# Kernel optimization log

Hardware: AMD Instinct MI355X
Metric: run time of the kernel (lower is better)

Reference implementation:

```python
import jax, jax.numpy as jnp
import numpy as np

CAPACITY = 8_388_608  # 2**23, power of two -> leftmost_leaf == capacity
N_UPDATES = 1_048_576  # 2**20


def setup_inputs() -> dict:
    key = jax.random.key(0)
    k1, k2, k3 = jax.random.split(key, 3)
    # Existing tree buffer; values[1] is root, values[CAPACITY:2*CAPACITY] are leaves.
    tree_values = jax.random.uniform(k1, (2 * CAPACITY,), dtype=jnp.float32)
    # Distinct leaf indices in [0, CAPACITY): torch scatter-assign with duplicate
    # indices is nondeterministic, so the meaningful case is distinct indices.
    indices = jax.random.permutation(k2, CAPACITY)[:N_UPDATES].astype(jnp.int32)
    values = jax.random.uniform(k3, (N_UPDATES,), dtype=jnp.float32)
    return {"tree_values": tree_values, "indices": indices, "values": values}


def reference(tree_values, indices, values):
    """SegmentTree.__setitem__ with op=add: set leaves, propagate sums to root.

    Returns the updated (2*capacity,) tree buffer.
    """
    capacity = tree_values.shape[0] // 2  # static python int
    depth = int(capacity).bit_length() - 1  # log2(capacity) levels to the root
    # _index_to_leaf: with power-of-two capacity, leaf = idx + capacity (no wrap).
    leaf = indices.astype(jnp.int32) + capacity
    tree = tree_values.at[leaf].set(values)
    idx = leaf
    # Original does torch.unique(idx//2) per level purely as an optimization;
    # duplicate parents recompute the identical value, so plain scatter-set of
    # op(left_child, right_child) is the same math and jit-friendly.
    for _ in range(depth):
        idx = idx // 2
        parent = tree[2 * idx] + tree[2 * idx + 1]
        tree = tree.at[idx].set(parent)
    return tree
```

## Files before the change

### kernel.cpp

```cpp
#include <hip/hip_runtime.h>


typedef unsigned int uint;
typedef unsigned char uchar;
typedef unsigned long long ull;

#define NBINS 4096
#define FCAP  512

__device__ __forceinline__ ull pc64(ull c) {
    ull x = (c | (c >> 1)) & 0x5555555555555555ull;
    x = (x | (x >> 1))  & 0x3333333333333333ull;
    x = (x | (x >> 2))  & 0x0F0F0F0F0F0F0F0Full;
    x = (x | (x >> 4))  & 0x00FF00FF00FF00FFull;
    x = (x | (x >> 8))  & 0x0000FFFF0000FFFFull;
    x = (x | (x >> 16)) & 0x00000000FFFFFFFFull;
    return x;
}

__global__ void clear_kernel(uint* __restrict__ fcnt) {
    fcnt[blockIdx.x * 256 + threadIdx.x] = 0u;
}

__global__ __launch_bounds__(1024)
void bin_kernel(const int* __restrict__ idx,
                const float* __restrict__ val,
                uint* __restrict__ fcnt,
                uint2* __restrict__ fbins) {
    __shared__ uint hist[NBINS];
    __shared__ uint rbase[NBINS];
    const int tid = threadIdx.x;

    #pragma unroll
    for (int e = 0; e < 4; ++e) hist[e * 1024 + tid] = 0u;
    __syncthreads();

    const int base4 = blockIdx.x * 1024 + tid;
    int4   j4 = ((const int4*)idx)[base4];
    float4 v4 = ((const float4*)val)[base4];
    uint  j[4] = { (uint)j4.x, (uint)j4.y, (uint)j4.z, (uint)j4.w };
    float v[4] = { v4.x, v4.y, v4.z, v4.w };

    #pragma unroll
    for (int e = 0; e < 4; ++e) atomicAdd(&hist[j[e] >> 11], 1u);
    __syncthreads();

    #pragma unroll
    for (int e = 0; e < 4; ++e) {
        int bin = e * 1024 + tid;
        uint h = hist[bin];
        rbase[bin] = h ? atomicAdd(&fcnt[bin], h) : 0u;
        hist[bin] = 0u;
    }
    __syncthreads();

    #pragma unroll
    for (int e = 0; e < 4; ++e) {
        uint bin = j[e] >> 11;
        uint r = rbase[bin] + atomicAdd(&hist[bin], 1u);
        if (r < FCAP)
            fbins[((size_t)bin << 9) + r] =
                make_uint2(j[e] & 2047u, __float_as_uint(v[e]));
    }
}

__global__ __launch_bounds__(256)
void merge_kernel(const float* __restrict__ tree,
                  const uint* __restrict__ fcnt,
                  const uint2* __restrict__ fbins,
                  uchar* __restrict__ l11flag,
                  float* __restrict__ out, int C) {
    __shared__ float slv[2048];
    __shared__ uchar sfl[2048];
    __shared__ float swv[4];
    __shared__ uint  swd[4];

    const int b   = blockIdx.x;
    const int tid = threadIdx.x;
    const int w    = tid >> 6;
    const int lane = tid & 63;

    ((uint2*)sfl)[tid] = make_uint2(0u, 0u);
    __syncthreads();
    uint c = fcnt[b];
    if (c > FCAP) c = FCAP;
    const uint2* mybin = fbins + ((size_t)b << 9);
    for (uint k = tid; k < c; k += 256u) {
        uint2 e = mybin[k];
        uint off = e.x & 2047u;
        slv[off] = __uint_as_float(e.y);
        sfl[off] = 1;
    }
    __syncthreads();

    const int leaf0  = tid * 8;
    const int gleaf0 = b * 2048 + leaf0;

    uint2 fw = *(const uint2*)&sfl[leaf0];
    float4 la = *(const float4*)&slv[leaf0];
    float4 lb = *(const float4*)&slv[leaf0 + 4];
    float4 ta = *(const float4*)(tree + C + gleaf0);
    float4 tb = *(const float4*)(tree + C + gleaf0 + 4);

    float l0 = (fw.x & 0x000000FFu) ? la.x : ta.x;
    float l1 = (fw.x & 0x0000FF00u) ? la.y : ta.y;
    float l2 = (fw.x & 0x00FF0000u) ? la.z : ta.z;
    float l3 = (fw.x & 0xFF000000u) ? la.w : ta.w;
    float l4 = (fw.y & 0x000000FFu) ? lb.x : tb.x;
    float l5 = (fw.y & 0x0000FF00u) ? lb.y : tb.y;
    float l6 = (fw.y & 0x00FF0000u) ? lb.z : tb.z;
    float l7 = (fw.y & 0xFF000000u) ? lb.w : tb.w;

    *(float4*)(out + C + gleaf0)     = make_float4(l0, l1, l2, l3);
    *(float4*)(out + C + gleaf0 + 4) = make_float4(l4, l5, l6, l7);

    uint d10 = (fw.x & 0x0000FFFFu) != 0u;
    uint d11 = (fw.x & 0xFFFF0000u) != 0u;
    uint d12 = (fw.y & 0x0000FFFFu) != 0u;
    uint d13 = (fw.y & 0xFFFF0000u) != 0u;
    float4 t1 = *(const float4*)(tree + (C >> 1) + (gleaf0 >> 1));
    float4 v1;
    v1.x = d10 ? l0 + l1 : t1.x;
    v1.y = d11 ? l2 + l3 : t1.y;
    v1.z = d12 ? l4 + l5 : t1.z;
    v1.w = d13 ? l6 + l7 : t1.w;
    *(float4*)(out + (C >> 1) + (gleaf0 >> 1)) = v1;

    float2 t2 = *(const float2*)(tree + (C >> 2) + (gleaf0 >> 2));
    uint d20 = d10 | d11, d21 = d12 | d13;
    float2 v2;
    v2.x = d20 ? v1.x + v1.y : t2.x;
    v2.y = d21 ? v1.z + v1.w : t2.y;
    *(float2*)(out + (C >> 2) + (gleaf0 >> 2)) = v2;

    float t3 = tree[(C >> 3) + (gleaf0 >> 3)];
    uint d3 = d20 | d21;
    float v = d3 ? v2.x + v2.y : t3;
    out[(C >> 3) + (gleaf0 >> 3)] = v;

    ull m = __ballot(d3 != 0u);
    #pragma unroll
    for (int lvl = 4; lvl <= 9; ++lvl) {
        float a  = __shfl(v, 2 * lane, 64);
        float bb = __shfl(v, 2 * lane + 1, 64);
        m = pc64(m);
        int n = 64 >> (lvl - 3);
        if (lane < n) {
            int node = (C >> lvl) + ((b * 2048 + w * 512) >> lvl) + lane;
            uint d = (uint)(m >> lane) & 1u;
            v = d ? a + bb : tree[node];
            out[node] = v;
        }
    }

    if (lane == 0) { swv[w] = v; swd[w] = (uint)(m & 1ull); }
    __syncthreads();
    if (tid == 0) {
        uint da0 = swd[0] | swd[1], da1 = swd[2] | swd[3];
        int n10 = (C >> 10) + 2 * b;
        float v100 = da0 ? swv[0] + swv[1] : tree[n10];
        float v101 = da1 ? swv[2] + swv[3] : tree[n10 + 1];
        out[n10]     = v100;
        out[n10 + 1] = v101;
        uint d11f = da0 | da1;
        int n11 = (C >> 11) + b;
        out[n11] = d11f ? v100 + v101 : tree[n11];
        l11flag[b] = (uchar)d11f;
    }
}

__global__ __launch_bounds__(1024)
void tail_kernel(const float* __restrict__ tree,
                 const uchar* __restrict__ l11flag,
                 float* __restrict__ out) {
    __shared__ float s16[16];
    __shared__ uint  sd16[16];
    const int t = threadIdx.x, w = t >> 6, lane = t & 63;

    float4 ch = *(const float4*)(out + 4096 + 4 * t);
    uint fl = ((const uint*)l11flag)[t];
    uint d0 = (fl & 0x0000FFFFu) != 0u;
    uint d1 = (fl & 0xFFFF0000u) != 0u;
    float2 t12 = *(const float2*)(tree + 2048 + 2 * t);
    float v0 = d0 ? ch.x + ch.y : t12.x;
    float v1 = d1 ? ch.z + ch.w : t12.y;
    *(float2*)(out + 2048 + 2 * t) = make_float2(v0, v1);
    uint d = d0 | d1;
    float v = d ? v0 + v1 : tree[1024 + t];
    out[1024 + t] = v;

    ull m = __ballot(d != 0u);
    #pragma unroll
    for (int M = 512; M >= 16; M >>= 1) {
        float a  = __shfl(v, 2 * lane, 64);
        float bb = __shfl(v, 2 * lane + 1, 64);
        m = pc64(m);
        int nw = M >> 4;
        if (lane < nw) {
            int node = M + nw * w + lane;
            uint dd = (uint)(m >> lane) & 1u;
            v = dd ? a + bb : tree[node];
            out[node] = v;
        }
    }
    if (lane == 0) { s16[w] = v; sd16[w] = (uint)(m & 1ull); }
    __syncthreads();

    if (w == 0) {
        float vv = lane < 16 ? s16[lane] : 0.f;
        uint dd  = lane < 16 ? sd16[lane] : 0u;
        ull mm = __ballot(dd != 0u);
        #pragma unroll
        for (int M = 8; M >= 1; M >>= 1) {
            float a  = __shfl(vv, 2 * lane, 64);
            float bb = __shfl(vv, 2 * lane + 1, 64);
            mm = pc64(mm);
            if (lane < M) {
                uint d2 = (uint)(mm >> lane) & 1u;
                vv = d2 ? a + bb : tree[M + lane];
                out[M + lane] = vv;
            }
        }
        if (lane == 0) out[0] = tree[0];
    }
}

extern "C" void kernel_launch(void* const* d_in, const int* in_sizes, int n_in,
                              void* d_out, int out_size, void* d_ws, size_t ws_size,
                              hipStream_t stream) {
    const float* tree    = (const float*)d_in[0];
    const int*   indices = (const int*)d_in[1];
    const float* values  = (const float*)d_in[2];
    float* out = (float*)d_out;

    const int two_cap = in_sizes[0];
    const int C       = two_cap >> 1;

    uchar* ws = (uchar*)d_ws;
    uint*  fcnt  = (uint*)ws;
    uchar* l11   = ws + 16384;
    uint2* fbins = (uint2*)(ws + 32768);

    clear_kernel<<<16, 256, 0, stream>>>(fcnt);
    bin_kernel<<<256, 1024, 0, stream>>>(indices, values, fcnt, fbins);
    merge_kernel<<<C / 2048, 256, 0, stream>>>(tree, fcnt, fbins, l11, out, C);
    tail_kernel<<<1, 1024, 0, stream>>>(tree, l11, out);
}
```

Before: 151.0 us.

## Fuse bin, merge and tail into one cooperative kernel with a bitmap

Replaces the clear/bin/merge/tail four-kernel pipeline with a single cooperative kernel that uses grid-wide syncs. Updates are scattered directly into the output leaves and recorded in a global dirty bitmap, which replaces the per-bin histogram and bucket staging. Leaf merging and upward propagation are then done per 512-leaf row, with block 0 finishing the top levels. This removes three kernel launches and the bucket buffer traffic, at the cost of grid.sync barriers, random scattered global writes, and only 256 blocks covering the whole 8M-leaf sweep.

```diff
diff --git a/kernel.cpp b/kernel.cpp
--- a/kernel.cpp
+++ b/kernel.cpp
@@ -1,12 +1,15 @@
 #include <hip/hip_runtime.h>
+#include <hip/hip_cooperative_groups.h>
+
+namespace cg = cooperative_groups;
 
 
 typedef unsigned int uint;
 typedef unsigned char uchar;
 typedef unsigned long long ull;
 
-#define NBINS 4096
-#define FCAP  512
+#define NBLK 256
+#define NTHR 1024
 
 __device__ __forceinline__ ull pc64(ull c) {
     ull x = (c | (c >> 1)) & 0x5555555555555555ull;
@@ -18,210 +21,192 @@
     return x;
 }
 
-__global__ void clear_kernel(uint* __restrict__ fcnt) {
-    fcnt[blockIdx.x * 256 + threadIdx.x] = 0u;
-}
-
-__global__ __launch_bounds__(1024)
-void bin_kernel(const int* __restrict__ idx,
-                const float* __restrict__ val,
-                uint* __restrict__ fcnt,
-                uint2* __restrict__ fbins) {
-    __shared__ uint hist[NBINS];
-    __shared__ uint rbase[NBINS];
-    const int tid = threadIdx.x;
-
-    #pragma unroll
-    for (int e = 0; e < 4; ++e) hist[e * 1024 + tid] = 0u;
-    __syncthreads();
-
-    const int base4 = blockIdx.x * 1024 + tid;
-    int4   j4 = ((const int4*)idx)[base4];
-    float4 v4 = ((const float4*)val)[base4];
-    uint  j[4] = { (uint)j4.x, (uint)j4.y, (uint)j4.z, (uint)j4.w };
-    float v[4] = { v4.x, v4.y, v4.z, v4.w };
-
-    #pragma unroll
-    for (int e = 0; e < 4; ++e) atomicAdd(&hist[j[e] >> 11], 1u);
-    __syncthreads();
-
-    #pragma unroll
-    for (int e = 0; e < 4; ++e) {
-        int bin = e * 1024 + tid;
-        uint h = hist[bin];
-        rbase[bin] = h ? atomicAdd(&fcnt[bin], h) : 0u;
-        hist[bin] = 0u;
+__global__ __launch_bounds__(NTHR)
+void fused_kernel(const float* __restrict__ tree,
+                  const int* __restrict__ idx,
+                  const float* __restrict__ val,
+                  uint* __restrict__ bitmap,
+                  uchar* __restrict__ l9flag,
+                  float* __restrict__ out,
+                  int C, int nupd) {
+    cg::grid_group grid = cg::this_grid();
+    const int tid  = threadIdx.x;
+    const int b    = blockIdx.x;
+    const int gtid = b * NTHR + tid;
+
+    if (gtid < (C >> 5)) bitmap[gtid] = 0u;
+    __threadfence();
+    grid.sync();
+
+    if (4 * gtid < nupd) {
+        int4   j4 = ((const int4*)idx)[gtid];
+        float4 v4 = ((const float4*)val)[gtid];
+        out[C + j4.x] = v4.x;
+        out[C + j4.y] = v4.y;
+        out[C + j4.z] = v4.z;
+        out[C + j4.w] = v4.w;
+        atomicOr(&bitmap[((uint)j4.x) >> 5], 1u << (((uint)j4.x) & 31u));
+        atomicOr(&bitmap[((uint)j4.y) >> 5], 1u << (((uint)j4.y) & 31u));
+        atomicOr(&bitmap[((uint)j4.z) >> 5], 1u << (((uint)j4.z) & 31u));
+        atomicOr(&bitmap[((uint)j4.w) >> 5], 1u << (((uint)j4.w) & 31u));
     }
-    __syncthreads();
-
-    #pragma unroll
-    for (int e = 0; e < 4; ++e) {
-        uint bin = j[e] >> 11;
-        uint r = rbase[bin] + atomicAdd(&hist[bin], 1u);
-        if (r < FCAP)
-            fbins[((size_t)bin << 9) + r] =
-                make_uint2(j[e] & 2047u, __float_as_uint(v[e]));
+    __threadfence();
+    grid.sync();
+
+    {
+        const int wv   = tid >> 6;
+        const int lane = tid & 63;
+        #pragma unroll
+        for (int it = 0; it < 4; ++it) {
+            const int r      = b * 64 + it * 16 + wv;
+            const int gleaf0 = r * 512 + lane * 8;
+            uint dm = (uint)((const uchar*)bitmap)[r * 64 + lane];
+
+            float4 ta = *(const float4*)(tree + C + gleaf0);
+            float4 tb = *(const float4*)(tree + C + gleaf0 + 4);
+            float4 oa = make_float4(0.f, 0.f, 0.f, 0.f), ob = oa;
+            if (dm) {
+                oa = *(const float4*)(out + C + gleaf0);
+                ob = *(const float4*)(out + C + gleaf0 + 4);
+            }
+            float l0 = (dm &   1u) ? oa.x : ta.x;
+            float l1 = (dm &   2u) ? oa.y : ta.y;
+            float l2 = (dm &   4u) ? oa.z : ta.z;
+            float l3 = (dm &   8u) ? oa.w : ta.w;
+            float l4 = (dm &  16u) ? ob.x : tb.x;
+            float l5 = (dm &  32u) ? ob.y : tb.y;
+            float l6 = (dm &  64u) ? ob.z : tb.z;
+            float l7 = (dm & 128u) ? ob.w : tb.w;
+            *(float4*)(out + C + gleaf0)     = make_float4(l0, l1, l2, l3);
+            *(float4*)(out + C + gleaf0 + 4) = make_float4(l4, l5, l6, l7);
+
+            uint d10 = dm & 3u, d11 = dm & 12u, d12 = dm & 48u, d13 = dm & 192u;
+            float4 t1 = *(const float4*)(tree + (C >> 1) + (gleaf0 >> 1));
+            float4 v1;
+            v1.x = d10 ? l0 + l1 : t1.x;
+            v1.y = d11 ? l2 + l3 : t1.y;
+            v1.z = d12 ? l4 + l5 : t1.z;
+            v1.w = d13 ? l6 + l7 : t1.w;
+            *(float4*)(out + (C >> 1) + (gleaf0 >> 1)) = v1;
+
+            float2 t2 = *(const float2*)(tree + (C >> 2) + (gleaf0 >> 2));
+            uint d20 = d10 | d11, d21 = d12 | d13;
+            float2 v2;
+            v2.x = d20 ? v1.x + v1.y : t2.x;
+            v2.y = d21 ? v1.z + v1.w : t2.y;
+            *(float2*)(out + (C >> 2) + (gleaf0 >> 2)) = v2;
+
+            float t3v = tree[(C >> 3) + (gleaf0 >> 3)];
+            uint d3 = d20 | d21;
+            float v = d3 ? v2.x + v2.y : t3v;
+            out[(C >> 3) + (gleaf0 >> 3)] = v;
+
+            ull m = __ballot(d3 != 0u);
+            #pragma unroll
+            for (int lvl = 4; lvl <= 9; ++lvl) {
+                float a  = __shfl(v, 2 * lane, 64);
+                float bb = __shfl(v, 2 * lane + 1, 64);
+                m = pc64(m);
+                int n = 64 >> (lvl - 3);
+                if (lane < n) {
+                    int node = (C >> lvl) + (r << (9 - lvl)) + lane;
+                    uint dd = (uint)(m >> lane) & 1u;
+                    v = dd ? a + bb : tree[node];
+                    out[node] = v;
+                }
+            }
+            if (lane == 0) l9flag[r] = (uchar)(m & 1ull);
+        }
     }
-}
-
-__global__ __launch_bounds__(256)
-void merge_kernel(const float* __restrict__ tree,
-                  const uint* __restrict__ fcnt,
-                  const uint2* __restrict__ fbins,
-                  uchar* __restrict__ l11flag,
-                  float* __restrict__ out, int C) {
-    __shared__ float slv[2048];
-    __shared__ uchar sfl[2048];
-    __shared__ float swv[4];
-    __shared__ uint  swd[4];
-
-    const int b   = blockIdx.x;
-    const int tid = threadIdx.x;
-    const int w    = tid >> 6;
-    const int lane = tid & 63;
-
-    ((uint2*)sfl)[tid] = make_uint2(0u, 0u);
-    __syncthreads();
-    uint c = fcnt[b];
-    if (c > FCAP) c = FCAP;
-    const uint2* mybin = fbins + ((size_t)b << 9);
-    for (uint k = tid; k < c; k += 256u) {
-        uint2 e = mybin[k];
-        uint off = e.x & 2047u;
-        slv[off] = __uint_as_float(e.y);
-        sfl[off] = 1;
-    }
-    __syncthreads();
-
-    const int leaf0  = tid * 8;
-    const int gleaf0 = b * 2048 + leaf0;
-
-    uint2 fw = *(const uint2*)&sfl[leaf0];
-    float4 la = *(const float4*)&slv[leaf0];
-    float4 lb = *(const float4*)&slv[leaf0 + 4];
-    float4 ta = *(const float4*)(tree + C + gleaf0);
-    float4 tb = *(const float4*)(tree + C + gleaf0 + 4);
-
-    float l0 = (fw.x & 0x000000FFu) ? la.x : ta.x;
-    float l1 = (fw.x & 0x0000FF00u) ? la.y : ta.y;
-    float l2 = (fw.x & 0x00FF0000u) ? la.z : ta.z;
-    float l3 = (fw.x & 0xFF000000u) ? la.w : ta.w;
-    float l4 = (fw.y & 0x000000FFu) ? lb.x : tb.x;
-    float l5 = (fw.y & 0x0000FF00u) ? lb.y : tb.y;
-    float l6 = (fw.y & 0x00FF0000u) ? lb.z : tb.z;
-    float l7 = (fw.y & 0xFF000000u) ? lb.w : tb.w;
-
-    *(float4*)(out + C + gleaf0)     = make_float4(l0, l1, l2, l3);
-    *(float4*)(out + C + gleaf0 + 4) = make_float4(l4, l5, l6, l7);
-
-    uint d10 = (fw.x & 0x0000FFFFu) != 0u;
-    uint d11 = (fw.x & 0xFFFF0000u) != 0u;
-    uint d12 = (fw.y & 0x0000FFFFu) != 0u;
-    uint d13 = (fw.y & 0xFFFF0000u) != 0u;
-    float4 t1 = *(const float4*)(tree + (C >> 1) + (gleaf0 >> 1));
-    float4 v1;
-    v1.x = d10 ? l0 + l1 : t1.x;
-    v1.y = d11 ? l2 + l3 : t1.y;
-    v1.z = d12 ? l4 + l5 : t1.z;
-    v1.w = d13 ? l6 + l7 : t1.w;
-    *(float4*)(out + (C >> 1) + (gleaf0 >> 1)) = v1;
-
-    float2 t2 = *(const float2*)(tree + (C >> 2) + (gleaf0 >> 2));
-    uint d20 = d10 | d11, d21 = d12 | d13;
-    float2 v2;
-    v2.x = d20 ? v1.x + v1.y : t2.x;
-    v2.y = d21 ? v1.z + v1.w : t2.y;
-    *(float2*)(out + (C >> 2) + (gleaf0 >> 2)) = v2;
-
-    float t3 = tree[(C >> 3) + (gleaf0 >> 3)];
-    uint d3 = d20 | d21;
-    float v = d3 ? v2.x + v2.y : t3;
-    out[(C >> 3) + (gleaf0 >> 3)] = v;
-
-    ull m = __ballot(d3 != 0u);
-    #pragma unroll
-    for (int lvl = 4; lvl <= 9; ++lvl) {
-        float a  = __shfl(v, 2 * lane, 64);
-        float bb = __shfl(v, 2 * lane + 1, 64);
-        m = pc64(m);
-        int n = 64 >> (lvl - 3);
-        if (lane < n) {
-            int node = (C >> lvl) + ((b * 2048 + w * 512) >> lvl) + lane;
-            uint d = (uint)(m >> lane) & 1u;
-            v = d ? a + bb : tree[node];
-            out[node] = v;
-        }
-    }
-
-    if (lane == 0) { swv[w] = v; swd[w] = (uint)(m & 1ull); }
-    __syncthreads();
-    if (tid == 0) {
-        uint da0 = swd[0] | swd[1], da1 = swd[2] | swd[3];
-        int n10 = (C >> 10) + 2 * b;
-        float v100 = da0 ? swv[0] + swv[1] : tree[n10];
-        float v101 = da1 ? swv[2] + swv[3] : tree[n10 + 1];
-        out[n10]     = v100;
-        out[n10 + 1] = v101;
-        uint d11f = da0 | da1;
-        int n11 = (C >> 11) + b;
-        out[n11] = d11f ? v100 + v101 : tree[n11];
-        l11flag[b] = (uchar)d11f;
-    }
-}
-
-__global__ __launch_bounds__(1024)
-void tail_kernel(const float* __restrict__ tree,
-                 const uchar* __restrict__ l11flag,
-                 float* __restrict__ out) {
-    __shared__ float s16[16];
-    __shared__ uint  sd16[16];
-    const int t = threadIdx.x, w = t >> 6, lane = t & 63;
-
-    float4 ch = *(const float4*)(out + 4096 + 4 * t);
-    uint fl = ((const uint*)l11flag)[t];
-    uint d0 = (fl & 0x0000FFFFu) != 0u;
-    uint d1 = (fl & 0xFFFF0000u) != 0u;
-    float2 t12 = *(const float2*)(tree + 2048 + 2 * t);
-    float v0 = d0 ? ch.x + ch.y : t12.x;
-    float v1 = d1 ? ch.z + ch.w : t12.y;
-    *(float2*)(out + 2048 + 2 * t) = make_float2(v0, v1);
-    uint d = d0 | d1;
-    float v = d ? v0 + v1 : tree[1024 + t];
-    out[1024 + t] = v;
-
-    ull m = __ballot(d != 0u);
-    #pragma unroll
-    for (int M = 512; M >= 16; M >>= 1) {
-        float a  = __shfl(v, 2 * lane, 64);
-        float bb = __shfl(v, 2 * lane + 1, 64);
-        m = pc64(m);
-        int nw = M >> 4;
-        if (lane < nw) {
-            int node = M + nw * w + lane;
-            uint dd = (uint)(m >> lane) & 1u;
-            v = dd ? a + bb : tree[node];
-            out[node] = v;
-        }
-    }
-    if (lane == 0) { s16[w] = v; sd16[w] = (uint)(m & 1ull); }
-    __syncthreads();
-
-    if (w == 0) {
-        float vv = lane < 16 ? s16[lane] : 0.f;
-        uint dd  = lane < 16 ? sd16[lane] : 0u;
-        ull mm = __ballot(dd != 0u);
-        #pragma unroll
-        for (int M = 8; M >= 1; M >>= 1) {
-            float a  = __shfl(vv, 2 * lane, 64);
-            float bb = __shfl(vv, 2 * lane + 1, 64);
-            mm = pc64(mm);
-            if (lane < M) {
-                uint d2 = (uint)(mm >> lane) & 1u;
-                vv = d2 ? a + bb : tree[M + lane];
-                out[M + lane] = vv;
-            }
-        }
-        if (lane == 0) out[0] = tree[0];
+    __threadfence();
+    grid.sync();
+
+    if (b == 0) {
+        __shared__ float s16v[16];
+        __shared__ uint  s16d[16];
+        const int t = tid, w = t >> 6, lane = t & 63;
+
+        const int L9 = C >> 9;
+        float s9[16];
+        *(float4*)&s9[0]  = *(const float4*)(out + L9 + 16 * t);
+        *(float4*)&s9[4]  = *(const float4*)(out + L9 + 16 * t + 4);
+        *(float4*)&s9[8]  = *(const float4*)(out + L9 + 16 * t + 8);
+        *(float4*)&s9[12] = *(const float4*)(out + L9 + 16 * t + 12);
+        uint4 fq = *(const uint4*)(l9flag + 16 * t);
+        uint f[4] = { fq.x, fq.y, fq.z, fq.w };
+
+        const int L10 = C >> 10;
+        float4 t10a = *(const float4*)(tree + L10 + 8 * t);
+        float4 t10b = *(const float4*)(tree + L10 + 8 * t + 4);
+        float t10_[8] = { t10a.x, t10a.y, t10a.z, t10a.w,
+                          t10b.x, t10b.y, t10b.z, t10b.w };
+        float v10[8]; uint d10_[8];
+        #pragma unroll
+        for (int k = 0; k < 8; ++k) {
+            uint hw = (f[k >> 1] >> ((k & 1) * 16)) & 0xFFFFu;
+            d10_[k] = hw != 0u;
+            v10[k]  = hw ? s9[2 * k] + s9[2 * k + 1] : t10_[k];
+        }
+        *(float4*)(out + L10 + 8 * t)     = make_float4(v10[0], v10[1], v10[2], v10[3]);
+        *(float4*)(out + L10 + 8 * t + 4) = make_float4(v10[4], v10[5], v10[6], v10[7]);
+
+        const int L11 = C >> 11;
+        float4 t11 = *(const float4*)(tree + L11 + 4 * t);
+        float t11_[4] = { t11.x, t11.y, t11.z, t11.w };
+        float v11[4]; uint d11_[4];
+        #pragma unroll
+        for (int k = 0; k < 4; ++k) {
+            uint d = d10_[2 * k] | d10_[2 * k + 1];
+            d11_[k] = d;
+            v11[k]  = d ? v10[2 * k] + v10[2 * k + 1] : t11_[k];
+        }
+        *(float4*)(out + L11 + 4 * t) = make_float4(v11[0], v11[1], v11[2], v11[3]);
+
+        const int L12 = C >> 12;
+        float2 t12v = *(const float2*)(tree + L12 + 2 * t);
+        uint dA = d11_[0] | d11_[1], dB = d11_[2] | d11_[3];
+        float vA = dA ? v11[0] + v11[1] : t12v.x;
+        float vB = dB ? v11[2] + v11[3] : t12v.y;
+        *(float2*)(out + L12 + 2 * t) = make_float2(vA, vB);
+
+        uint d = dA | dB;
+        float v = d ? vA + vB : tree[(C >> 13) + t];
+        out[(C >> 13) + t] = v;
+
+        ull m = __ballot(d != 0u);
+        #pragma unroll
+        for (int M = 512; M >= 16; M >>= 1) {
+            float a  = __shfl(v, 2 * lane, 64);
+            float bb = __shfl(v, 2 * lane + 1, 64);
+            m = pc64(m);
+            int nw = M >> 4;
+            if (lane < nw) {
+                int node = M + nw * w + lane;
+                uint dd = (uint)(m >> lane) & 1u;
+                v = dd ? a + bb : tree[node];
+                out[node] = v;
+            }
+        }
+        if (lane == 0) { s16v[w] = v; s16d[w] = (uint)(m & 1ull); }
+        __syncthreads();
+
+        if (w == 0) {
+            float vv = lane < 16 ? s16v[lane] : 0.f;
+            uint dd  = lane < 16 ? s16d[lane] : 0u;
+            ull mm = __ballot(dd != 0u);
+            #pragma unroll
+            for (int M = 8; M >= 1; M >>= 1) {
+                float a  = __shfl(vv, 2 * lane, 64);
+                float bb = __shfl(vv, 2 * lane + 1, 64);
+                mm = pc64(mm);
+                if (lane < M) {
+                    uint d2 = (uint)(mm >> lane) & 1u;
+                    vv = d2 ? a + bb : tree[M + lane];
+                    out[M + lane] = vv;
+                }
+            }
+            if (lane == 0) out[0] = tree[0];
+        }
     }
 }
 
@@ -234,15 +219,23 @@
     float* out = (float*)d_out;
 
     const int two_cap = in_sizes[0];
-    const int C       = two_cap >> 1;
+    int C    = two_cap >> 1;
+    int nupd = in_sizes[1];
 
     uchar* ws = (uchar*)d_ws;
-    uint*  fcnt  = (uint*)ws;
-    uchar* l11   = ws + 16384;
-    uint2* fbins = (uint2*)(ws + 32768);
-
-    clear_kernel<<<16, 256, 0, stream>>>(fcnt);
-    bin_kernel<<<256, 1024, 0, stream>>>(indices, values, fcnt, fbins);
-    merge_kernel<<<C / 2048, 256, 0, stream>>>(tree, fcnt, fbins, l11, out, C);
-    tail_kernel<<<1, 1024, 0, stream>>>(tree, l11, out);
+    uint*  bitmap = (uint*)ws;
+    uchar* l9f    = ws + (1 << 20);
+
+    void* args[8];
+    args[0] = (void*)&tree;
+    args[1] = (void*)&indices;
+    args[2] = (void*)&values;
+    args[3] = (void*)&bitmap;
+    args[4] = (void*)&l9f;
+    args[5] = (void*)&out;
+    args[6] = (void*)&C;
+    args[7] = (void*)&nupd;
+
+    hipLaunchCooperativeKernel((const void*)fused_kernel,
+                               dim3(NBLK), dim3(NTHR), args, 0, stream);
 }
```

Measured after the change: 544.3 us. 3.61x slower.

## Enlarge merge tiles to 8192 leaves and fold upper levels into merge

Applied to the files above, without the earlier changes.

Each merge block now covers 8192 leaves with 1024 threads, so there are 1024 bins, each holding up to 2048 entries. The merge kernel reduces levels 10 through 13 in-block with a second wave-shuffle stage, which leaves the tail kernel only the top 10 levels. The clear kernel is replaced by hipMemsetAsync. The goal is fewer blocks, fewer per-bin atomics and less tail work, at the cost of larger shared memory per block (about 40KB), which may reduce occupancy.

```diff
diff --git a/kernel.cpp b/kernel.cpp
--- a/kernel.cpp
+++ b/kernel.cpp
@@ -5,8 +5,8 @@
 typedef unsigned char uchar;
 typedef unsigned long long ull;
 
-#define NBINS 4096
-#define FCAP  512
+#define NBINS 1024
+#define BCAP  2048
 
 __device__ __forceinline__ ull pc64(ull c) {
     ull x = (c | (c >> 1)) & 0x5555555555555555ull;
@@ -18,83 +18,72 @@
     return x;
 }
 
-__global__ void clear_kernel(uint* __restrict__ fcnt) {
-    fcnt[blockIdx.x * 256 + threadIdx.x] = 0u;
-}
-
 __global__ __launch_bounds__(1024)
 void bin_kernel(const int* __restrict__ idx,
                 const float* __restrict__ val,
-                uint* __restrict__ fcnt,
-                uint2* __restrict__ fbins) {
+                uint* __restrict__ cnt,
+                uint2* __restrict__ bins) {
     __shared__ uint hist[NBINS];
     __shared__ uint rbase[NBINS];
     const int tid = threadIdx.x;
-
-    #pragma unroll
-    for (int e = 0; e < 4; ++e) hist[e * 1024 + tid] = 0u;
-    __syncthreads();
-
-    const int base4 = blockIdx.x * 1024 + tid;
-    int4   j4 = ((const int4*)idx)[base4];
-    float4 v4 = ((const float4*)val)[base4];
+    hist[tid] = 0u;
+    __syncthreads();
+
+    const int g = blockIdx.x * 1024 + tid;
+    int4   j4 = ((const int4*)idx)[g];
+    float4 v4 = ((const float4*)val)[g];
     uint  j[4] = { (uint)j4.x, (uint)j4.y, (uint)j4.z, (uint)j4.w };
     float v[4] = { v4.x, v4.y, v4.z, v4.w };
 
     #pragma unroll
-    for (int e = 0; e < 4; ++e) atomicAdd(&hist[j[e] >> 11], 1u);
+    for (int e = 0; e < 4; ++e) atomicAdd(&hist[j[e] >> 13], 1u);
+    __syncthreads();
+
+    uint h = hist[tid];
+    rbase[tid] = h ? atomicAdd(&cnt[tid], h) : 0u;
+    hist[tid] = 0u;
     __syncthreads();
 
     #pragma unroll
     for (int e = 0; e < 4; ++e) {
-        int bin = e * 1024 + tid;
-        uint h = hist[bin];
-        rbase[bin] = h ? atomicAdd(&fcnt[bin], h) : 0u;
-        hist[bin] = 0u;
-    }
-    __syncthreads();
-
-    #pragma unroll
-    for (int e = 0; e < 4; ++e) {
-        uint bin = j[e] >> 11;
+        uint bin = j[e] >> 13;
         uint r = rbase[bin] + atomicAdd(&hist[bin], 1u);
-        if (r < FCAP)
-            fbins[((size_t)bin << 9) + r] =
-                make_uint2(j[e] & 2047u, __float_as_uint(v[e]));
-    }
-}
-
-__global__ __launch_bounds__(256)
+        if (r < BCAP)
+            bins[((size_t)bin << 11) + r] =
+                make_uint2(j[e] & 8191u, __float_as_uint(v[e]));
+    }
+}
+
+__global__ __launch_bounds__(1024)
 void merge_kernel(const float* __restrict__ tree,
-                  const uint* __restrict__ fcnt,
-                  const uint2* __restrict__ fbins,
-                  uchar* __restrict__ l11flag,
+                  const uint* __restrict__ cnt,
+                  const uint2* __restrict__ bins,
+                  uchar* __restrict__ l13flag,
                   float* __restrict__ out, int C) {
-    __shared__ float slv[2048];
-    __shared__ uchar sfl[2048];
-    __shared__ float swv[4];
-    __shared__ uint  swd[4];
-
-    const int b   = blockIdx.x;
-    const int tid = threadIdx.x;
-    const int w    = tid >> 6;
+    __shared__ float slv[8192];
+    __shared__ uchar sfl[8192];
+    __shared__ float s9v[16];
+    __shared__ uint  s9d[16];
+
+    const int b    = blockIdx.x;
+    const int tid  = threadIdx.x;
+    const int wv   = tid >> 6;
     const int lane = tid & 63;
 
     ((uint2*)sfl)[tid] = make_uint2(0u, 0u);
     __syncthreads();
-    uint c = fcnt[b];
-    if (c > FCAP) c = FCAP;
-    const uint2* mybin = fbins + ((size_t)b << 9);
-    for (uint k = tid; k < c; k += 256u) {
+    uint c = cnt[b];
+    if (c > BCAP) c = BCAP;
+    const uint2* mybin = bins + ((size_t)b << 11);
+    for (uint k = tid; k < c; k += 1024u) {
         uint2 e = mybin[k];
-        uint off = e.x & 2047u;
-        slv[off] = __uint_as_float(e.y);
-        sfl[off] = 1;
+        slv[e.x] = __uint_as_float(e.y);
+        sfl[e.x] = 1;
     }
     __syncthreads();
 
     const int leaf0  = tid * 8;
-    const int gleaf0 = b * 2048 + leaf0;
+    const int gleaf0 = b * 8192 + leaf0;
 
     uint2 fw = *(const uint2*)&sfl[leaf0];
     float4 la = *(const float4*)&slv[leaf0];
@@ -133,11 +122,12 @@
     v2.y = d21 ? v1.z + v1.w : t2.y;
     *(float2*)(out + (C >> 2) + (gleaf0 >> 2)) = v2;
 
-    float t3 = tree[(C >> 3) + (gleaf0 >> 3)];
+    float t3v = tree[(C >> 3) + (gleaf0 >> 3)];
     uint d3 = d20 | d21;
-    float v = d3 ? v2.x + v2.y : t3;
+    float v = d3 ? v2.x + v2.y : t3v;
     out[(C >> 3) + (gleaf0 >> 3)] = v;
 
+    const int r = b * 16 + wv;
     ull m = __ballot(d3 != 0u);
     #pragma unroll
     for (int lvl = 4; lvl <= 9; ++lvl) {
@@ -146,48 +136,46 @@
         m = pc64(m);
         int n = 64 >> (lvl - 3);
         if (lane < n) {
-            int node = (C >> lvl) + ((b * 2048 + w * 512) >> lvl) + lane;
-            uint d = (uint)(m >> lane) & 1u;
-            v = d ? a + bb : tree[node];
+            int node = (C >> lvl) + (r << (9 - lvl)) + lane;
+            uint dd = (uint)(m >> lane) & 1u;
+            v = dd ? a + bb : tree[node];
             out[node] = v;
         }
     }
-
-    if (lane == 0) { swv[w] = v; swd[w] = (uint)(m & 1ull); }
-    __syncthreads();
-    if (tid == 0) {
-        uint da0 = swd[0] | swd[1], da1 = swd[2] | swd[3];
-        int n10 = (C >> 10) + 2 * b;
-        float v100 = da0 ? swv[0] + swv[1] : tree[n10];
-        float v101 = da1 ? swv[2] + swv[3] : tree[n10 + 1];
-        out[n10]     = v100;
-        out[n10 + 1] = v101;
-        uint d11f = da0 | da1;
-        int n11 = (C >> 11) + b;
-        out[n11] = d11f ? v100 + v101 : tree[n11];
-        l11flag[b] = (uchar)d11f;
+    if (lane == 0) { s9v[wv] = v; s9d[wv] = (uint)(m & 1ull); }
+    __syncthreads();
+
+    if (wv == 0) {
+        float vv = lane < 16 ? s9v[lane] : 0.f;
+        uint dd  = lane < 16 ? s9d[lane] : 0u;
+        ull mm = __ballot(dd != 0u);
+        #pragma unroll
+        for (int lvl = 10; lvl <= 13; ++lvl) {
+            float a  = __shfl(vv, 2 * lane, 64);
+            float bb = __shfl(vv, 2 * lane + 1, 64);
+            mm = pc64(mm);
+            int n = 1 << (13 - lvl);
+            if (lane < n) {
+                int node = (C >> lvl) + (b << (13 - lvl)) + lane;
+                uint d2 = (uint)(mm >> lane) & 1u;
+                vv = d2 ? a + bb : tree[node];
+                out[node] = vv;
+            }
+        }
+        if (lane == 0) l13flag[b] = (uchar)(mm & 1ull);
     }
 }
 
 __global__ __launch_bounds__(1024)
 void tail_kernel(const float* __restrict__ tree,
-                 const uchar* __restrict__ l11flag,
+                 const uchar* __restrict__ l13flag,
                  float* __restrict__ out) {
-    __shared__ float s16[16];
-    __shared__ uint  sd16[16];
+    __shared__ float s16v[16];
+    __shared__ uint  s16d[16];
     const int t = threadIdx.x, w = t >> 6, lane = t & 63;
 
-    float4 ch = *(const float4*)(out + 4096 + 4 * t);
-    uint fl = ((const uint*)l11flag)[t];
-    uint d0 = (fl & 0x0000FFFFu) != 0u;
-    uint d1 = (fl & 0xFFFF0000u) != 0u;
-    float2 t12 = *(const float2*)(tree + 2048 + 2 * t);
-    float v0 = d0 ? ch.x + ch.y : t12.x;
-    float v1 = d1 ? ch.z + ch.w : t12.y;
-    *(float2*)(out + 2048 + 2 * t) = make_float2(v0, v1);
-    uint d = d0 | d1;
-    float v = d ? v0 + v1 : tree[1024 + t];
-    out[1024 + t] = v;
+    float v = out[1024 + t];
+    uint d = l13flag[t];
 
     ull m = __ballot(d != 0u);
     #pragma unroll
@@ -203,12 +191,12 @@
             out[node] = v;
         }
     }
-    if (lane == 0) { s16[w] = v; sd16[w] = (uint)(m & 1ull); }
+    if (lane == 0) { s16v[w] = v; s16d[w] = (uint)(m & 1ull); }
     __syncthreads();
 
     if (w == 0) {
-        float vv = lane < 16 ? s16[lane] : 0.f;
-        uint dd  = lane < 16 ? sd16[lane] : 0u;
+        float vv = lane < 16 ? s16v[lane] : 0.f;
+        uint dd  = lane < 16 ? s16d[lane] : 0u;
         ull mm = __ballot(dd != 0u);
         #pragma unroll
         for (int M = 8; M >= 1; M >>= 1) {
@@ -235,14 +223,15 @@
 
     const int two_cap = in_sizes[0];
     const int C       = two_cap >> 1;
+    const int nupd    = in_sizes[1];
 
     uchar* ws = (uchar*)d_ws;
-    uint*  fcnt  = (uint*)ws;
-    uchar* l11   = ws + 16384;
-    uint2* fbins = (uint2*)(ws + 32768);
-
-    clear_kernel<<<16, 256, 0, stream>>>(fcnt);
-    bin_kernel<<<256, 1024, 0, stream>>>(indices, values, fcnt, fbins);
-    merge_kernel<<<C / 2048, 256, 0, stream>>>(tree, fcnt, fbins, l11, out, C);
-    tail_kernel<<<1, 1024, 0, stream>>>(tree, l11, out);
-}
+    uint*  cnt  = (uint*)ws;
+    uchar* l13  = ws + 4096;
+    uint2* bins = (uint2*)(ws + 32768);
+
+    hipMemsetAsync(cnt, 0, NBINS * sizeof(uint), stream);
+    bin_kernel<<<nupd / 4096, 1024, 0, stream>>>(indices, values, cnt, bins);
+    merge_kernel<<<C / 8192, 1024, 0, stream>>>(tree, cnt, bins, l13, out, C);
+    tail_kernel<<<1, 1024, 0, stream>>>(tree, l13, out);
+}
```

Result: faster. 146.0 us (-3.3%).
